# Kernel tuning notes

Measured on AMD Instinct MI355X. Metric: run time of the kernel, lower is better.

The kernel has to match this reference:

```python
import jax, jax.numpy as jnp
import numpy as np

# 2^22-point radix-2 DIT FFT; NOTE the original code applies tf.abs at EVERY
# recursion level (not just the top), so each butterfly stage is followed by a
# magnitude + recomplexification. We reproduce that exact (non-standard) math.
N = 1 << 22
STAGES = 22


def _bitrev_perm(n, bits):
    # vectorized bit-reversal permutation (the order induced by the even/odd
    # decimation inputs[0::2] / inputs[1::2] recursion)
    x = np.arange(n)
    r = np.zeros(n, dtype=np.int64)
    for b in range(bits):
        r = (r << 1) | ((x >> b) & 1)
    return r


_PERM = jnp.asarray(_bitrev_perm(N, STAGES))


def setup_inputs() -> dict:
    key = jax.random.key(0)
    x = jax.random.normal(key, (N,), dtype=jnp.float32)
    return {"x": x}


def reference(x):
    # base case of the recursion: length-1 leaves are the bit-reversed inputs
    y = x[_PERM].astype(jnp.complex64)
    for s in range(1, STAGES + 1):  # fixed log2(N) stages, not a data loop
        m = 1 << s                  # sub-FFT size at this stage
        yb = y.reshape(N // m, m)   # [num_blocks, m]
        e = yb[:, : m // 2]         # 'even' sub-results
        o = yb[:, m // 2:]          # 'odd'  sub-results
        # twiddles W(m, k) = exp(-2*pi*i*k/m)
        tw = jnp.exp(
            jnp.complex64(-2j * np.pi) * jnp.arange(m // 2, dtype=jnp.float32) / m
        ).astype(jnp.complex64)
        t = tw[None, :] * o
        # butterfly then tf.abs (applied at every level in the original)
        mag = jnp.abs(jnp.concatenate([e + t, e - t], axis=1)).reshape(N)
        y = mag.astype(jnp.complex64) if s < STAGES else mag
    return y  # float32 magnitudes, shape [N]
```

## Files before the change

### kernel.cpp

```cpp
#include <hip/hip_runtime.h>
#include <math.h>


#define NBITS 22

__device__ __forceinline__ void bf(float& e, float& o, float c, float s) {
    float co = c * o, im = s * o;
    float rp = e + co, rm = e - co;
    float im2 = im * im;
    e = __builtin_amdgcn_sqrtf(fmaf(rp, rp, im2));
    o = __builtin_amdgcn_sqrtf(fmaf(rm, rm, im2));
}

__device__ __forceinline__ void cs(float r, float& c, float& s) {
    c = __builtin_amdgcn_cosf(r);
    s = __builtin_amdgcn_sinf(r);
}

__device__ __forceinline__ void radix8(float v[8], float b0, float b1, float b2) {
    float c, s;
    cs(b0, c, s);
    bf(v[0], v[1], c, s); bf(v[2], v[3], c, s);
    bf(v[4], v[5], c, s); bf(v[6], v[7], c, s);
    cs(b1, c, s);
    bf(v[0], v[2], c, s); bf(v[4], v[6], c, s);
    cs(b1 + 0.25f, c, s);
    bf(v[1], v[3], c, s); bf(v[5], v[7], c, s);
    cs(b2, c, s);           bf(v[0], v[4], c, s);
    cs(b2 + 0.125f, c, s);  bf(v[1], v[5], c, s);
    cs(b2 + 0.25f, c, s);   bf(v[2], v[6], c, s);
    cs(b2 + 0.375f, c, s);  bf(v[3], v[7], c, s);
}

#define PAD(i) ((i) + ((i) >> 3))

__global__ __launch_bounds__(256) void fft_perm(const float* __restrict__ x,
                                                float* __restrict__ y) {
    __shared__ float lds[64 * 65];
    const unsigned tid = threadIdx.x;
    const unsigned tx = tid & 63, g = tid >> 6;
    const unsigned C0 = (blockIdx.x & 31) * 64;
    const unsigned B0 = (blockIdx.x >> 5) * 64;

#pragma unroll
    for (int k = 0; k < 16; ++k) {
        unsigned r = g * 16 + k;
        unsigned a = __brev(C0 + r) >> (32 - 11);
        lds[r * 65 + tx] = x[a * 2048u + B0 + tx];
    }
    __syncthreads();

    float v[8];
#pragma unroll
    for (int q = 0; q < 2; ++q) {
        unsigned task = tid + 256u * q;
        unsigned c = task >> 3, grp = task & 7;
#pragma unroll
        for (int j = 0; j < 8; ++j) v[j] = lds[(grp * 8 + j) * 65 + c];
        radix8(v, 0.f, 0.f, 0.f);
        unsigned pr = __brev(B0 + c) >> (32 - 11);
        float* dst = y + pr * 2048u + C0 + grp * 8;
        *(float4*)(dst)     = make_float4(v[0], v[1], v[2], v[3]);
        *(float4*)(dst + 4) = make_float4(v[4], v[5], v[6], v[7]);
    }
}

__global__ __launch_bounds__(1024, 4) void fft_low(float* __restrict__ y) {
    __shared__ float lds[9216];
    const unsigned t = threadIdx.x;
    const unsigned base = blockIdx.x * 8192;
    float v[8];

    const float4* src = (const float4*)(y + base + t * 8);
    float4 u0 = src[0], u1 = src[1];
    v[0] = u0.x; v[1] = u0.y; v[2] = u0.z; v[3] = u0.w;
    v[4] = u1.x; v[5] = u1.y; v[6] = u1.z; v[7] = u1.w;
#pragma unroll
    for (int j = 0; j < 8; ++j) lds[PAD(t * 8 + j)] = v[j];
    __syncthreads();

    {
        const unsigned lo = t & 7, hi = t >> 3;
        const unsigned i0 = hi * 64 + lo;
#pragma unroll
        for (int j = 0; j < 8; ++j) v[j] = lds[PAD(i0 + j * 8)];
        const float f = (float)lo;
        radix8(v, f * (1.f/16), f * (1.f/32), f * (1.f/64));
#pragma unroll
        for (int j = 0; j < 8; ++j) lds[PAD(i0 + j * 8)] = v[j];
    }
    __syncthreads();

    {
        const unsigned lo = t & 63, hi = t >> 6;
        const unsigned i0 = hi * 512 + lo;
#pragma unroll
        for (int j = 0; j < 8; ++j) v[j] = lds[PAD(i0 + j * 64)];
        const float f = (float)lo;
        radix8(v, f * (1.f/128), f * (1.f/256), f * (1.f/512));
#pragma unroll
        for (int j = 0; j < 8; ++j) lds[PAD(i0 + j * 64)] = v[j];
    }
    __syncthreads();

    {
        const unsigned lo = t & 511, hi = t >> 9;
        const unsigned i0 = hi * 4096 + lo;
#pragma unroll
        for (int j = 0; j < 8; ++j) v[j] = lds[PAD(i0 + j * 512)];
        const float f = (float)lo;
        radix8(v, f * (1.f/1024), f * (1.f/2048), f * (1.f/4096));
#pragma unroll
        for (int j = 0; j < 8; ++j) lds[PAD(i0 + j * 512)] = v[j];
    }
    __syncthreads();

#pragma unroll
    for (int it = 0; it < 4; ++it) {
        const unsigned i = it * 1024 + t;
        float e = lds[PAD(i)];
        float o = lds[PAD(i + 4096)];
        float c, s;
        cs((float)i * (1.f/8192), c, s);
        bf(e, o, c, s);
        y[base + i] = e;
        y[base + i + 4096] = o;
    }
}

__global__ __launch_bounds__(1024, 4) void fft_high(float* __restrict__ y) {
    __shared__ float lds[512 * 17 + 16];
    const unsigned tt = threadIdx.x;
    const unsigned li = tt & 15, u = tt >> 4;
    const unsigned low = blockIdx.x * 16 + li;
    float v[8];

#pragma unroll
    for (int j = 0; j < 8; ++j) v[j] = y[low + 8192u * (u * 8 + j)];
    {
        const float K = (float)low;
        radix8(v, K * (1.f/16384), K * (1.f/32768), K * (1.f/65536));
    }
#pragma unroll
    for (int j = 0; j < 8; ++j) lds[(u * 8 + j) * 17 + li] = v[j];
    __syncthreads();

    {
        const unsigned lo8 = u & 7, hi = u >> 3;
        const unsigned t0 = hi * 64 + lo8;
#pragma unroll
        for (int j = 0; j < 8; ++j) v[j] = lds[(t0 + j * 8) * 17 + li];
        const float K = (float)low + 8192.f * (float)lo8;
        radix8(v, K * (1.f/131072), K * (1.f/262144), K * (1.f/524288));
#pragma unroll
        for (int j = 0; j < 8; ++j) lds[(t0 + j * 8) * 17 + li] = v[j];
    }
    __syncthreads();

    {
#pragma unroll
        for (int j = 0; j < 8; ++j) v[j] = lds[(u + j * 64) * 17 + li];
        const float K = (float)low + 8192.f * (float)u;
        radix8(v, K * (1.f/1048576), K * (1.f/2097152), K * (1.f/4194304));
#pragma unroll
        for (int j = 0; j < 8; ++j) y[low + 8192u * (u + j * 64)] = v[j];
    }
}

extern "C" void kernel_launch(void* const* d_in, const int* in_sizes, int n_in,
                              void* d_out, int out_size, void* d_ws, size_t ws_size,
                              hipStream_t stream) {
    const float* x = (const float*)d_in[0];
    float* out = (float*)d_out;

    fft_perm<<<dim3(1024), dim3(256), 0, stream>>>(x, out);
    fft_low<<<dim3(512), dim3(1024), 0, stream>>>(out);
    fft_high<<<dim3(512), dim3(1024), 0, stream>>>(out);
}
```

Baseline: 101.2 us.

## Derive radix-8 twiddles algebraically and specialize zero-twiddle first stages

Replaces the per-butterfly hardware sin/cos calls with a single sin/cos per radix-8 group, deriving the other twiddles by double-angle identities and 45-degree rotations. The first three stages in fft_perm use specialized butterflies (abs of sum/difference, shared magnitude) because their twiddles are trivial. fft_low's LDS staging switches to float4 stores with a different padding scheme, its final stage rotates the twiddle recurrently, and the occupancy hints are raised to 8 blocks. This cuts transcendental and ALU work but may add rounding error from the recurrences, and the higher launch bounds may squeeze registers.

```diff
diff --git a/kernel.cpp b/kernel.cpp
--- a/kernel.cpp
+++ b/kernel.cpp
@@ -3,39 +3,57 @@
 
 
 #define NBITS 22
+#define RSQ2 0.70710678118654752440f
+
+__device__ __forceinline__ float hsqrt(float x) { return __builtin_amdgcn_sqrtf(x); }
 
 __device__ __forceinline__ void bf(float& e, float& o, float c, float s) {
-    float co = c * o, im = s * o;
-    float rp = e + co, rm = e - co;
+    float rp = fmaf(c, o, e);
+    float rm = fmaf(-c, o, e);
+    float im = s * o;
     float im2 = im * im;
-    e = __builtin_amdgcn_sqrtf(fmaf(rp, rp, im2));
-    o = __builtin_amdgcn_sqrtf(fmaf(rm, rm, im2));
-}
-
-__device__ __forceinline__ void cs(float r, float& c, float& s) {
-    c = __builtin_amdgcn_cosf(r);
-    s = __builtin_amdgcn_sinf(r);
-}
-
-__device__ __forceinline__ void radix8(float v[8], float b0, float b1, float b2) {
-    float c, s;
-    cs(b0, c, s);
-    bf(v[0], v[1], c, s); bf(v[2], v[3], c, s);
-    bf(v[4], v[5], c, s); bf(v[6], v[7], c, s);
-    cs(b1, c, s);
-    bf(v[0], v[2], c, s); bf(v[4], v[6], c, s);
-    cs(b1 + 0.25f, c, s);
-    bf(v[1], v[3], c, s); bf(v[5], v[7], c, s);
-    cs(b2, c, s);           bf(v[0], v[4], c, s);
-    cs(b2 + 0.125f, c, s);  bf(v[1], v[5], c, s);
-    cs(b2 + 0.25f, c, s);   bf(v[2], v[6], c, s);
-    cs(b2 + 0.375f, c, s);  bf(v[3], v[7], c, s);
-}
-
-#define PAD(i) ((i) + ((i) >> 3))
-
-__global__ __launch_bounds__(256) void fft_perm(const float* __restrict__ x,
-                                                float* __restrict__ y) {
+    e = hsqrt(fmaf(rp, rp, im2));
+    o = hsqrt(fmaf(rm, rm, im2));
+}
+__device__ __forceinline__ void bf0(float& e, float& o) {
+    float a = e + o, b = e - o;
+    e = fabsf(a); o = fabsf(b);
+}
+__device__ __forceinline__ void bfq(float& e, float& o) {
+    float h = hsqrt(fmaf(e, e, o * o));
+    e = h; o = h;
+}
+
+__device__ __forceinline__ void radix8f(float v[8], float c2, float s2) {
+    float c1 = fmaf(-2.f * s2, s2, 1.f);
+    float s1 = 2.f * s2 * c2;
+    float c0 = fmaf(-2.f * s1, s1, 1.f);
+    float s0 = 2.f * s1 * c1;
+    bf(v[0], v[1], c0, s0); bf(v[2], v[3], c0, s0);
+    bf(v[4], v[5], c0, s0); bf(v[6], v[7], c0, s0);
+    bf(v[0], v[2], c1, s1); bf(v[4], v[6], c1, s1);
+    bf(v[1], v[3], -s1, c1); bf(v[5], v[7], -s1, c1);
+    bf(v[0], v[4], c2, s2);
+    float u = RSQ2 * (c2 - s2), w = RSQ2 * (c2 + s2);
+    bf(v[1], v[5], u, w);
+    bf(v[2], v[6], -s2, c2);
+    bf(v[3], v[7], -w, u);
+}
+
+__device__ __forceinline__ void radix8z(float v[8]) {
+    bf0(v[0], v[1]); bf0(v[2], v[3]); bf0(v[4], v[5]); bf0(v[6], v[7]);
+    bf0(v[0], v[2]); bf0(v[4], v[6]);
+    bfq(v[1], v[3]); bfq(v[5], v[7]);
+    bf0(v[0], v[4]);
+    bf(v[1], v[5], RSQ2, RSQ2);
+    bfq(v[2], v[6]);
+    bf(v[3], v[7], -RSQ2, RSQ2);
+}
+
+#define PAD32(i) ((i) + (((i) >> 5) << 2))
+
+__global__ __launch_bounds__(256, 8) void fft_perm(const float* __restrict__ x,
+                                                   float* __restrict__ y) {
     __shared__ float lds[64 * 65];
     const unsigned tid = threadIdx.x;
     const unsigned tx = tid & 63, g = tid >> 6;
@@ -57,7 +75,7 @@
         unsigned c = task >> 3, grp = task & 7;
 #pragma unroll
         for (int j = 0; j < 8; ++j) v[j] = lds[(grp * 8 + j) * 65 + c];
-        radix8(v, 0.f, 0.f, 0.f);
+        radix8z(v);
         unsigned pr = __brev(B0 + c) >> (32 - 11);
         float* dst = y + pr * 2048u + C0 + grp * 8;
         *(float4*)(dst)     = make_float4(v[0], v[1], v[2], v[3]);
@@ -65,29 +83,30 @@
     }
 }
 
-__global__ __launch_bounds__(1024, 4) void fft_low(float* __restrict__ y) {
+__global__ __launch_bounds__(1024, 8) void fft_low(float* __restrict__ y) {
     __shared__ float lds[9216];
     const unsigned t = threadIdx.x;
     const unsigned base = blockIdx.x * 8192;
     float v[8];
 
-    const float4* src = (const float4*)(y + base + t * 8);
-    float4 u0 = src[0], u1 = src[1];
-    v[0] = u0.x; v[1] = u0.y; v[2] = u0.z; v[3] = u0.w;
-    v[4] = u1.x; v[5] = u1.y; v[6] = u1.z; v[7] = u1.w;
-#pragma unroll
-    for (int j = 0; j < 8; ++j) lds[PAD(t * 8 + j)] = v[j];
+    {
+        const float4* src = (const float4*)(y + base + t * 8);
+        float4 u0 = src[0], u1 = src[1];
+        float* dst = &lds[PAD32(t * 8)];
+        ((float4*)dst)[0] = u0;
+        ((float4*)dst)[1] = u1;
+    }
     __syncthreads();
 
     {
         const unsigned lo = t & 7, hi = t >> 3;
         const unsigned i0 = hi * 64 + lo;
 #pragma unroll
-        for (int j = 0; j < 8; ++j) v[j] = lds[PAD(i0 + j * 8)];
-        const float f = (float)lo;
-        radix8(v, f * (1.f/16), f * (1.f/32), f * (1.f/64));
-#pragma unroll
-        for (int j = 0; j < 8; ++j) lds[PAD(i0 + j * 8)] = v[j];
+        for (int j = 0; j < 8; ++j) v[j] = lds[PAD32(i0 + j * 8)];
+        float r = (float)lo * (1.f / 64);
+        radix8f(v, __builtin_amdgcn_cosf(r), __builtin_amdgcn_sinf(r));
+#pragma unroll
+        for (int j = 0; j < 8; ++j) lds[PAD32(i0 + j * 8)] = v[j];
     }
     __syncthreads();
 
@@ -95,11 +114,11 @@
         const unsigned lo = t & 63, hi = t >> 6;
         const unsigned i0 = hi * 512 + lo;
 #pragma unroll
-        for (int j = 0; j < 8; ++j) v[j] = lds[PAD(i0 + j * 64)];
-        const float f = (float)lo;
-        radix8(v, f * (1.f/128), f * (1.f/256), f * (1.f/512));
-#pragma unroll
-        for (int j = 0; j < 8; ++j) lds[PAD(i0 + j * 64)] = v[j];
+        for (int j = 0; j < 8; ++j) v[j] = lds[PAD32(i0 + j * 64)];
+        float r = (float)lo * (1.f / 512);
+        radix8f(v, __builtin_amdgcn_cosf(r), __builtin_amdgcn_sinf(r));
+#pragma unroll
+        for (int j = 0; j < 8; ++j) lds[PAD32(i0 + j * 64)] = v[j];
     }
     __syncthreads();
 
@@ -107,28 +126,33 @@
         const unsigned lo = t & 511, hi = t >> 9;
         const unsigned i0 = hi * 4096 + lo;
 #pragma unroll
-        for (int j = 0; j < 8; ++j) v[j] = lds[PAD(i0 + j * 512)];
-        const float f = (float)lo;
-        radix8(v, f * (1.f/1024), f * (1.f/2048), f * (1.f/4096));
-#pragma unroll
-        for (int j = 0; j < 8; ++j) lds[PAD(i0 + j * 512)] = v[j];
-    }
-    __syncthreads();
-
-#pragma unroll
-    for (int it = 0; it < 4; ++it) {
-        const unsigned i = it * 1024 + t;
-        float e = lds[PAD(i)];
-        float o = lds[PAD(i + 4096)];
-        float c, s;
-        cs((float)i * (1.f/8192), c, s);
-        bf(e, o, c, s);
-        y[base + i] = e;
-        y[base + i + 4096] = o;
-    }
-}
-
-__global__ __launch_bounds__(1024, 4) void fft_high(float* __restrict__ y) {
+        for (int j = 0; j < 8; ++j) v[j] = lds[PAD32(i0 + j * 512)];
+        float r = (float)lo * (1.f / 4096);
+        radix8f(v, __builtin_amdgcn_cosf(r), __builtin_amdgcn_sinf(r));
+#pragma unroll
+        for (int j = 0; j < 8; ++j) lds[PAD32(i0 + j * 512)] = v[j];
+    }
+    __syncthreads();
+
+    {
+        float c = __builtin_amdgcn_cosf((float)t * (1.f / 8192));
+        float s = __builtin_amdgcn_sinf((float)t * (1.f / 8192));
+#pragma unroll
+        for (int it = 0; it < 4; ++it) {
+            const unsigned i = it * 1024 + t;
+            float e = lds[PAD32(i)];
+            float o = lds[PAD32(i + 4096)];
+            bf(e, o, c, s);
+            y[base + i] = e;
+            y[base + i + 4096] = o;
+            float nc = RSQ2 * (c - s);
+            s = RSQ2 * (c + s);
+            c = nc;
+        }
+    }
+}
+
+__global__ __launch_bounds__(1024, 8) void fft_high(float* __restrict__ y) {
     __shared__ float lds[512 * 17 + 16];
     const unsigned tt = threadIdx.x;
     const unsigned li = tt & 15, u = tt >> 4;
@@ -138,8 +162,8 @@
 #pragma unroll
     for (int j = 0; j < 8; ++j) v[j] = y[low + 8192u * (u * 8 + j)];
     {
-        const float K = (float)low;
-        radix8(v, K * (1.f/16384), K * (1.f/32768), K * (1.f/65536));
+        float r = (float)low * (1.f / 65536);
+        radix8f(v, __builtin_amdgcn_cosf(r), __builtin_amdgcn_sinf(r));
     }
 #pragma unroll
     for (int j = 0; j < 8; ++j) lds[(u * 8 + j) * 17 + li] = v[j];
@@ -150,8 +174,8 @@
         const unsigned t0 = hi * 64 + lo8;
 #pragma unroll
         for (int j = 0; j < 8; ++j) v[j] = lds[(t0 + j * 8) * 17 + li];
-        const float K = (float)low + 8192.f * (float)lo8;
-        radix8(v, K * (1.f/131072), K * (1.f/262144), K * (1.f/524288));
+        float r = ((float)low + 8192.f * (float)lo8) * (1.f / 524288);
+        radix8f(v, __builtin_amdgcn_cosf(r), __builtin_amdgcn_sinf(r));
 #pragma unroll
         for (int j = 0; j < 8; ++j) lds[(t0 + j * 8) * 17 + li] = v[j];
     }
@@ -160,8 +184,8 @@
     {
 #pragma unroll
         for (int j = 0; j < 8; ++j) v[j] = lds[(u + j * 64) * 17 + li];
-        const float K = (float)low + 8192.f * (float)u;
-        radix8(v, K * (1.f/1048576), K * (1.f/2097152), K * (1.f/4194304));
+        float r = ((float)low + 8192.f * (float)u) * (1.f / 4194304);
+        radix8f(v, __builtin_amdgcn_cosf(r), __builtin_amdgcn_sinf(r));
 #pragma unroll
         for (int j = 0; j < 8; ++j) y[low + 8192u * (u + j * 64)] = v[j];
     }
```

After: 103.4 us. 1.02x slower.
